# Optimization experiments

Measured on AMD Instinct MI355X. Metric: run time of the kernel, lower is better.

The kernel has to match this reference:

```python
import jax, jax.numpy as jnp
import numpy as np

B, T, F, U = 64, 1024, 128, 256


def setup_inputs() -> dict:
    key = jax.random.key(0)
    k1, k2, k3 = jax.random.split(key, 3)
    inputs = jax.random.normal(k1, (B, T, F), dtype=jnp.float32)
    # R ~ Normal(stddev=1/time_horizon)
    R = jax.random.normal(k2, (F, U), dtype=jnp.float32) / T
    # W ~ Orthogonal init
    a = jax.random.normal(k3, (U, U), dtype=jnp.float32)
    q, r = jnp.linalg.qr(a)
    W = q * jnp.sign(jnp.diag(r))[None, :]
    bias = jnp.zeros((U,), dtype=jnp.float32)
    x0 = jnp.zeros((U,), dtype=jnp.float32)
    return {"inputs": inputs, "R": R, "W": W, "bias": bias, "x0": x0}


def reference(inputs, R, W, bias, x0):
    # inputs: [B, T, F]. Precompute input projections for all steps at once.
    h_all = jnp.einsum("btf,fu->tbu", inputs, R)  # [T, B, U]
    state0 = jnp.broadcast_to(x0, (inputs.shape[0], x0.shape[0]))  # [B, U]

    def step(state, h):
        new_state = jnp.tanh(h + state @ W + bias)
        return new_state, new_state

    _, states = jax.lax.scan(step, state0, h_all)  # states: [T, B, U]
    return states
```

## Files before the change

### kernel.cpp

```cpp
#include <hip/hip_runtime.h>
#include <hip/hip_bf16.h>

constexpr int B = 64;
constexpr int T = 1024;
constexpr int F = 128;
constexpr int U = 256;
constexpr int CH = 8;

__device__ __forceinline__ float toF32(float v) { return v; }
__device__ __forceinline__ float toF32(__hip_bfloat16 v) { return __bfloat162float(v); }

__device__ __forceinline__ void store8(float* p, const float* a) {
    ((float4*)p)[0] = make_float4(a[0], a[1], a[2], a[3]);
    ((float4*)p)[1] = make_float4(a[4], a[5], a[6], a[7]);
}
__device__ __forceinline__ void store8(__hip_bfloat16* p, const float* a) {
    unsigned int v[4];
    #pragma unroll
    for (int i = 0; i < 4; ++i) {
        __hip_bfloat16 lo = __float2bfloat16(a[2 * i]);
        __hip_bfloat16 hi = __float2bfloat16(a[2 * i + 1]);
        unsigned short lob = *(unsigned short*)&lo;
        unsigned short hib = *(unsigned short*)&hi;
        v[i] = (unsigned int)lob | ((unsigned int)hib << 16);
    }
    ((uint4*)p)[0] = make_uint4(v[0], v[1], v[2], v[3]);
}

__device__ __forceinline__ float rdlane(float v, int l) {
    return __uint_as_float(__builtin_amdgcn_readlane(__float_as_uint(v), l));
}

__device__ __forceinline__ float tanh_fast(float x) {
    float e = __builtin_amdgcn_exp2f(x * 2.885390081777927f);
    float r = __builtin_amdgcn_rcpf(1.0f + e);
    return fmaf(-2.0f, r, 1.0f);
}

__device__ __forceinline__ void lds_barrier() {
    __builtin_amdgcn_s_waitcnt(0xC07F);
    asm volatile("" ::: "memory");
    __builtin_amdgcn_s_barrier();
    asm volatile("" ::: "memory");
}

template <typename HT>
__global__ __launch_bounds__(512, 2) void proj_kernel(
    const float* __restrict__ in,
    const float* __restrict__ Rm,
    HT* __restrict__ h)
{
    const int t0   = blockIdx.x * 64;
    const int u0b  = blockIdx.y * 64;
    const int b    = blockIdx.z;
    const int tid  = threadIdx.x;
    const int lane = tid & 63;
    const int wv   = tid >> 6;
    const int u0   = __builtin_amdgcn_readfirstlane(u0b + wv * 8);

    __shared__ float4 a4[64 * 32];

    const float4* src = (const float4*)(in + ((size_t)b * T + t0) * F);
    #pragma unroll
    for (int it = 0; it < 4; ++it) {
        int f  = tid + it * 512;
        int r  = f >> 5;
        int k4 = f & 31;
        a4[(r << 5) | (k4 ^ (r & 31))] = src[f];
    }
    __syncthreads();

    const float* Rp = Rm + u0;
    float acc[8];
    #pragma unroll
    for (int j = 0; j < 8; ++j) acc[j] = 0.f;

    float ra[32], rb[32];
    #pragma unroll
    for (int kk = 0; kk < 4; ++kk)
        #pragma unroll
        for (int j = 0; j < 8; ++j)
            ra[kk * 8 + j] = Rp[(size_t)kk * U + j];

    const int r = lane;
    #pragma unroll
    for (int k4 = 0; k4 < 32; k4 += 2) {
        #pragma unroll
        for (int kk = 0; kk < 4; ++kk)
            #pragma unroll
            for (int j = 0; j < 8; ++j)
                rb[kk * 8 + j] = Rp[(size_t)((k4 + 1) * 4 + kk) * U + j];

        float4 av = a4[(r << 5) | (k4 ^ (r & 31))];
        #pragma unroll
        for (int j = 0; j < 8; ++j) {
            acc[j] = fmaf(av.x, ra[0 * 8 + j], acc[j]);
            acc[j] = fmaf(av.y, ra[1 * 8 + j], acc[j]);
            acc[j] = fmaf(av.z, ra[2 * 8 + j], acc[j]);
            acc[j] = fmaf(av.w, ra[3 * 8 + j], acc[j]);
        }

        if (k4 + 2 < 32) {
            #pragma unroll
            for (int kk = 0; kk < 4; ++kk)
                #pragma unroll
                for (int j = 0; j < 8; ++j)
                    ra[kk * 8 + j] = Rp[(size_t)((k4 + 2) * 4 + kk) * U + j];
        }

        float4 av2 = a4[(r << 5) | ((k4 + 1) ^ (r & 31))];
        #pragma unroll
        for (int j = 0; j < 8; ++j) {
            acc[j] = fmaf(av2.x, rb[0 * 8 + j], acc[j]);
            acc[j] = fmaf(av2.y, rb[1 * 8 + j], acc[j]);
            acc[j] = fmaf(av2.z, rb[2 * 8 + j], acc[j]);
            acc[j] = fmaf(av2.w, rb[3 * 8 + j], acc[j]);
        }
    }

    HT* hp = h + ((size_t)(t0 + r) * B + b) * U + u0;
    store8(hp, acc);
}

template <typename HT>
__global__ __launch_bounds__(512, 2) void rnn_kernel(
    const HT* __restrict__ h,
    const float* __restrict__ Wm,
    const float* __restrict__ bias,
    const float* __restrict__ x0,
    float* __restrict__ out)
{
    const int b    = blockIdx.x;
    const int tid  = threadIdx.x;
    const int l    = tid & 63;
    const int wv   = tid >> 6;
    const int k0   = wv << 5;

    __shared__ float p[2][8][256];

    float w0[32], w1[32], w2[32], w3[32];
    {
        const float* wp = Wm + (size_t)k0 * U + 4 * l;
        #pragma unroll
        for (int kk = 0; kk < 32; ++kk) {
            float4 v = *(const float4*)(wp + (size_t)kk * U);
            w0[kk] = v.x; w1[kk] = v.y; w2[kk] = v.z; w3[kk] = v.w;
        }
    }

    const bool act = (l < 32);
    const int  u   = k0 + (l & 31);
    const float bv = bias[u];

    float tv = x0[u];

    const size_t sT = (size_t)B * U;
    const HT* hp = h + (size_t)b * U + u;
    float* op = out + (size_t)b * U + u;

    float hc[CH], hn[CH], ob[CH];
    #pragma unroll
    for (int i = 0; i < CH; ++i) hc[i] = toF32(hp[(size_t)i * sT]);

    for (int tc = 0; tc < T; tc += CH) {
        if (tc + CH < T) {
            #pragma unroll
            for (int i = 0; i < CH; ++i)
                hn[i] = toF32(hp[(size_t)(tc + CH + i) * sT]);
        }
        if (tc > 0 && act) {
            #pragma unroll
            for (int i = 0; i < CH; ++i)
                op[(size_t)(tc - CH + i) * sT] = ob[i];
        }

        #pragma unroll
        for (int i = 0; i < CH; ++i) {
            float sb[32];
            #pragma unroll
            for (int kk = 0; kk < 32; ++kk) sb[kk] = rdlane(tv, kk);

            float a0 = 0.f, a1 = 0.f, a2 = 0.f, a3 = 0.f;
            #pragma unroll
            for (int kk = 0; kk < 32; ++kk) {
                a0 = fmaf(sb[kk], w0[kk], a0);
                a1 = fmaf(sb[kk], w1[kk], a1);
                a2 = fmaf(sb[kk], w2[kk], a2);
                a3 = fmaf(sb[kk], w3[kk], a3);
            }
            *(float4*)&p[i & 1][wv][4 * l] = make_float4(a0, a1, a2, a3);

            lds_barrier();

            float red = p[i & 1][0][u];
            #pragma unroll
            for (int w2i = 1; w2i < 8; ++w2i) red += p[i & 1][w2i][u];

            float val = tanh_fast(red + hc[i] + bv);
            ob[i] = val;
            tv = val;
        }

        if (tc + CH < T) {
            #pragma unroll
            for (int i = 0; i < CH; ++i) hc[i] = hn[i];
        }
    }

    if (act) {
        #pragma unroll
        for (int i = 0; i < CH; ++i)
            op[(size_t)(T - CH + i) * sT] = ob[i];
    }
}

extern "C" void kernel_launch(void* const* d_in, const int* in_sizes, int n_in,
                              void* d_out, int out_size, void* d_ws, size_t ws_size,
                              hipStream_t stream) {
    const float* in   = (const float*)d_in[0];
    const float* Rm   = (const float*)d_in[1];
    const float* Wm   = (const float*)d_in[2];
    const float* bias = (const float*)d_in[3];
    const float* x0   = (const float*)d_in[4];
    float* out = (float*)d_out;

    const size_t hElems = (size_t)T * B * U;
    dim3 pgrid(T / 64, U / 64, B);

    if (ws_size >= hElems * sizeof(float)) {
        float* h = (float*)d_ws;
        proj_kernel<float><<<pgrid, 512, 0, stream>>>(in, Rm, h);
        rnn_kernel<float><<<dim3(B), 512, 0, stream>>>(h, Wm, bias, x0, out);
    } else {
        __hip_bfloat16* h = (__hip_bfloat16*)d_ws;
        proj_kernel<__hip_bfloat16><<<pgrid, 512, 0, stream>>>(in, Rm, h);
        rnn_kernel<__hip_bfloat16><<<dim3(B), 512, 0, stream>>>(h, Wm, bias, x0, out);
    }
}
```

Before: 674.1 us.

## Use packed fp16 dot2 for recurrent matvec with 4-wave blocks and DPP reduction

The recurrent kernel now keeps W in registers as packed fp16 pairs and computes the state@W product with v_dot2 instructions, which halves the number of arithmetic instructions per step. The block drops from 8 waves to 4, each wave covering 64 input rows. The cross-wave partial sums are read back from LDS and reduced across lanes with DPP row shifts, and each owner lane produces and stores 4 outputs as float4. The goal is to shorten the serial per-step critical path (readlanes, FMAs, barrier cost with fewer waves). The trade-off is that the hidden state and W are rounded to fp16, which costs accuracy.

```diff
diff --git a/kernel.cpp b/kernel.cpp
--- a/kernel.cpp
+++ b/kernel.cpp
@@ -5,10 +5,9 @@
 constexpr int T = 1024;
 constexpr int F = 128;
 constexpr int U = 256;
-constexpr int CH = 8;
-
-__device__ __forceinline__ float toF32(float v) { return v; }
-__device__ __forceinline__ float toF32(__hip_bfloat16 v) { return __bfloat162float(v); }
+constexpr int CH = 4;
+
+typedef _Float16 h2 __attribute__((ext_vector_type(2)));
 
 __device__ __forceinline__ void store8(float* p, const float* a) {
     ((float4*)p)[0] = make_float4(a[0], a[1], a[2], a[3]);
@@ -27,8 +26,23 @@
     ((uint4*)p)[0] = make_uint4(v[0], v[1], v[2], v[3]);
 }
 
-__device__ __forceinline__ float rdlane(float v, int l) {
-    return __uint_as_float(__builtin_amdgcn_readlane(__float_as_uint(v), l));
+template <typename HT> struct HRawT;
+template <> struct HRawT<float>           { using T = float4;  };
+template <> struct HRawT<__hip_bfloat16>  { using T = ushort4; };
+
+__device__ __forceinline__ float4 toF4(float4 v) { return v; }
+__device__ __forceinline__ float4 toF4(ushort4 v) {
+    float4 r;
+    r.x = __uint_as_float((unsigned)v.x << 16);
+    r.y = __uint_as_float((unsigned)v.y << 16);
+    r.z = __uint_as_float((unsigned)v.z << 16);
+    r.w = __uint_as_float((unsigned)v.w << 16);
+    return r;
+}
+
+__device__ __forceinline__ unsigned pack_rn(float a, float b) {
+    h2 p = { (_Float16)a, (_Float16)b };
+    return __builtin_bit_cast(unsigned, p);
 }
 
 __device__ __forceinline__ float tanh_fast(float x) {
@@ -42,6 +56,12 @@
     asm volatile("" ::: "memory");
     __builtin_amdgcn_s_barrier();
     asm volatile("" ::: "memory");
+}
+
+template <int CTRL>
+__device__ __forceinline__ float dpp_add(float x) {
+    int sh = __builtin_amdgcn_update_dpp(0, __float_as_int(x), CTRL, 0xF, 0xF, true);
+    return x + __int_as_float(sh);
 }
 
 template <typename HT>
@@ -123,94 +143,128 @@
 }
 
 template <typename HT>
-__global__ __launch_bounds__(512, 2) void rnn_kernel(
+__global__ __launch_bounds__(256, 1) void rnn_kernel(
     const HT* __restrict__ h,
     const float* __restrict__ Wm,
     const float* __restrict__ bias,
     const float* __restrict__ x0,
     float* __restrict__ out)
 {
-    const int b    = blockIdx.x;
-    const int tid  = threadIdx.x;
-    const int l    = tid & 63;
-    const int wv   = tid >> 6;
-    const int k0   = wv << 5;
-
-    __shared__ float p[2][8][256];
-
-    float w0[32], w1[32], w2[32], w3[32];
+    using Raw = typename HRawT<HT>::T;
+
+    const int b   = blockIdx.x;
+    const int tid = threadIdx.x;
+    const int l   = tid & 63;
+    const int wv  = tid >> 6;
+    const int k0  = wv << 6;
+    const int q   = l >> 2;
+    const int w2  = l & 3;
+    const int ub  = k0 + 4 * q;
+    const bool owner = (w2 == 3);
+
+    __shared__ float pp[2][4 * 264];
+
+    h2 wp0[32], wp1[32], wp2[32], wp3[32];
     {
-        const float* wp = Wm + (size_t)k0 * U + 4 * l;
+        const float* wb = Wm + (size_t)k0 * U + 4 * l;
         #pragma unroll
         for (int kk = 0; kk < 32; ++kk) {
-            float4 v = *(const float4*)(wp + (size_t)kk * U);
-            w0[kk] = v.x; w1[kk] = v.y; w2[kk] = v.z; w3[kk] = v.w;
-        }
-    }
-
-    const bool act = (l < 32);
-    const int  u   = k0 + (l & 31);
-    const float bv = bias[u];
-
-    float tv = x0[u];
+            float4 r0 = *(const float4*)(wb + (size_t)(2 * kk) * U);
+            float4 r1 = *(const float4*)(wb + (size_t)(2 * kk + 1) * U);
+            wp0[kk] = h2{ (_Float16)r0.x, (_Float16)r1.x };
+            wp1[kk] = h2{ (_Float16)r0.y, (_Float16)r1.y };
+            wp2[kk] = h2{ (_Float16)r0.z, (_Float16)r1.z };
+            wp3[kk] = h2{ (_Float16)r0.w, (_Float16)r1.w };
+        }
+    }
+
+    float4 sv = *(const float4*)(x0 + ub);
+    unsigned spA = pack_rn(sv.x, sv.y);
+    unsigned spB = pack_rn(sv.z, sv.w);
+
+    const float4 bv = *(const float4*)(bias + ub);
 
     const size_t sT = (size_t)B * U;
-    const HT* hp = h + (size_t)b * U + u;
-    float* op = out + (size_t)b * U + u;
-
-    float hc[CH], hn[CH], ob[CH];
-    #pragma unroll
-    for (int i = 0; i < CH; ++i) hc[i] = toF32(hp[(size_t)i * sT]);
+    const HT* hp = h + (size_t)b * U + ub;
+    float* op = out + (size_t)b * U + ub;
+
+    Raw hcr[CH], hnr[CH];
+    float4 ob[CH];
+    #pragma unroll
+    for (int i = 0; i < CH; ++i)
+        hcr[i] = *(const Raw*)(hp + (size_t)i * sT);
 
     for (int tc = 0; tc < T; tc += CH) {
         if (tc + CH < T) {
             #pragma unroll
             for (int i = 0; i < CH; ++i)
-                hn[i] = toF32(hp[(size_t)(tc + CH + i) * sT]);
-        }
-        if (tc > 0 && act) {
+                hnr[i] = *(const Raw*)(hp + (size_t)(tc + CH + i) * sT);
+        }
+        if (tc > 0 && owner) {
             #pragma unroll
             for (int i = 0; i < CH; ++i)
-                op[(size_t)(tc - CH + i) * sT] = ob[i];
+                *(float4*)(op + (size_t)(tc - CH + i) * sT) = ob[i];
         }
 
         #pragma unroll
         for (int i = 0; i < CH; ++i) {
-            float sb[32];
-            #pragma unroll
-            for (int kk = 0; kk < 32; ++kk) sb[kk] = rdlane(tv, kk);
+            unsigned sb[32];
+            #pragma unroll
+            for (int kk = 0; kk < 32; ++kk)
+                sb[kk] = __builtin_amdgcn_readlane((kk & 1) ? spB : spA,
+                                                   4 * (kk >> 1) + 3);
 
             float a0 = 0.f, a1 = 0.f, a2 = 0.f, a3 = 0.f;
-            #pragma unroll
-            for (int kk = 0; kk < 32; ++kk) {
-                a0 = fmaf(sb[kk], w0[kk], a0);
-                a1 = fmaf(sb[kk], w1[kk], a1);
-                a2 = fmaf(sb[kk], w2[kk], a2);
-                a3 = fmaf(sb[kk], w3[kk], a3);
+            float a4 = 0.f, a5 = 0.f, a6 = 0.f, a7 = 0.f;
+            #pragma unroll
+            for (int kk = 0; kk < 32; kk += 2) {
+                h2 s0 = __builtin_bit_cast(h2, sb[kk]);
+                h2 s1 = __builtin_bit_cast(h2, sb[kk + 1]);
+                a0 = __builtin_amdgcn_fdot2(wp0[kk], s0, a0, false);
+                a1 = __builtin_amdgcn_fdot2(wp1[kk], s0, a1, false);
+                a2 = __builtin_amdgcn_fdot2(wp2[kk], s0, a2, false);
+                a3 = __builtin_amdgcn_fdot2(wp3[kk], s0, a3, false);
+                a4 = __builtin_amdgcn_fdot2(wp0[kk + 1], s1, a4, false);
+                a5 = __builtin_amdgcn_fdot2(wp1[kk + 1], s1, a5, false);
+                a6 = __builtin_amdgcn_fdot2(wp2[kk + 1], s1, a6, false);
+                a7 = __builtin_amdgcn_fdot2(wp3[kk + 1], s1, a7, false);
             }
-            *(float4*)&p[i & 1][wv][4 * l] = make_float4(a0, a1, a2, a3);
+
+            const int par = i & 1;
+            *(float4*)&pp[par][wv * 264 + 4 * l] =
+                make_float4(a0 + a4, a1 + a5, a2 + a6, a3 + a7);
 
             lds_barrier();
 
-            float red = p[i & 1][0][u];
-            #pragma unroll
-            for (int w2i = 1; w2i < 8; ++w2i) red += p[i & 1][w2i][u];
-
-            float val = tanh_fast(red + hc[i] + bv);
+            float4 rp = *(const float4*)&pp[par][w2 * 264 + ub];
+
+            rp.x = dpp_add<0x112>(dpp_add<0x111>(rp.x));
+            rp.y = dpp_add<0x112>(dpp_add<0x111>(rp.y));
+            rp.z = dpp_add<0x112>(dpp_add<0x111>(rp.z));
+            rp.w = dpp_add<0x112>(dpp_add<0x111>(rp.w));
+
+            float4 hv = toF4(hcr[i]);
+            float4 val;
+            val.x = tanh_fast(rp.x + hv.x + bv.x);
+            val.y = tanh_fast(rp.y + hv.y + bv.y);
+            val.z = tanh_fast(rp.z + hv.z + bv.z);
+            val.w = tanh_fast(rp.w + hv.w + bv.w);
             ob[i] = val;
-            tv = val;
+
+            spA = pack_rn(val.x, val.y);
+            spB = pack_rn(val.z, val.w);
         }
 
         if (tc + CH < T) {
             #pragma unroll
-            for (int i = 0; i < CH; ++i) hc[i] = hn[i];
-        }
-    }
-
-    if (act) {
+            for (int i = 0; i < CH; ++i) hcr[i] = hnr[i];
+        }
+    }
+
+    if (owner) {
         #pragma unroll
         for (int i = 0; i < CH; ++i)
-            op[(size_t)(T - CH + i) * sT] = ob[i];
+            *(float4*)(op + (size_t)(T - CH + i) * sT) = ob[i];
     }
 }
 
@@ -230,10 +284,10 @@
     if (ws_size >= hElems * sizeof(float)) {
         float* h = (float*)d_ws;
         proj_kernel<float><<<pgrid, 512, 0, stream>>>(in, Rm, h);
-        rnn_kernel<float><<<dim3(B), 512, 0, stream>>>(h, Wm, bias, x0, out);
+        rnn_kernel<float><<<dim3(B), 256, 0, stream>>>(h, Wm, bias, x0, out);
     } else {
         __hip_bfloat16* h = (__hip_bfloat16*)d_ws;
         proj_kernel<__hip_bfloat16><<<pgrid, 512, 0, stream>>>(in, Rm, h);
-        rnn_kernel<__hip_bfloat16><<<dim3(B), 512, 0, stream>>>(h, Wm, bias, x0, out);
-    }
-}
+        rnn_kernel<__hip_bfloat16><<<dim3(B), 256, 0, stream>>>(h, Wm, bias, x0, out);
+    }
+}
```

Result: no change. 684.2 us (+1.5%).
